# Kernel optimization log

Measured on AMD Instinct MI355X. Metric: run time of the kernel, lower is better.

## Reference

```python
import jax, jax.numpy as jnp
import numpy as np


def _att(xf, W1, W2):
    # xf: [B, L, dk]; low-rank attention scores, softmax over last dim
    dk = W1.shape[0]
    s1 = xf @ W1                                   # [B, L, 10]
    s2 = jnp.einsum('rk,bjk->brj', W2, xf)         # [B, 10, L]
    scores = jnp.einsum('bir,brj->bij', s1, s2) / jnp.sqrt(jnp.float32(dk))
    return jax.nn.softmax(scores, axis=-1)         # [B, L, L]


def setup_inputs() -> dict:
    B, Ci, Co, N, T = 8, 64, 64, 1000, 24
    ks = jax.random.split(jax.random.key(0), 16)
    f32 = jnp.float32
    return {
        'x': jax.random.normal(ks[0], (B, Ci, N, T), f32),
        'A_adj': jax.random.uniform(ks[1], (N, N), f32),
        'att0_W1': jax.random.normal(ks[2], (N * T, 10), f32) * 0.02,
        'att0_W2': jax.random.normal(ks[3], (10, N * T), f32) * 0.02,
        'gatt_W1': jax.random.normal(ks[4], (Ci * T, 10), f32) * 0.02,
        'gatt_W2': jax.random.normal(ks[5], (10, Ci * T), f32) * 0.02,
        'gcn_W': jax.random.normal(ks[6], (Ci, Co), f32) * 0.05,
        'tatt_W1': jax.random.normal(ks[7], (N * Co, 10), f32) * 0.02,
        'tatt_W2': jax.random.normal(ks[8], (10, N * Co), f32) * 0.02,
        'conv1_w': jax.random.normal(ks[9], (Co, Co, 1, 2), f32) * 0.05,
        'conv1_b': jax.random.normal(ks[10], (Co,), f32) * 0.05,
        'conv2_w': jax.random.normal(ks[11], (Co, Co, 1, 2), f32) * 0.05,
        'conv2_b': jax.random.normal(ks[12], (Co,), f32) * 0.05,
        'res_w': jax.random.normal(ks[13], (Co, Ci, 1, 1), f32) * 0.05,
        'res_b': jax.random.normal(ks[14], (Co,), f32) * 0.05,
        'ln_g': jnp.ones((Co,), f32),
        'ln_b': jnp.zeros((Co,), f32),
    }


def reference(x, A_adj, att0_W1, att0_W2, gatt_W1, gatt_W2, gcn_W,
              tatt_W1, tatt_W2, conv1_w, conv1_b, conv2_w, conv2_b,
              res_w, res_b, ln_g, ln_b):
    B, C, N, T = x.shape
    # ---- block-level channel attention (requires_value=True) ----
    xf = x.reshape(B, C, N * T)
    x1 = (_att(xf, att0_W1, att0_W2) @ xf).reshape(B, C, N, T)
    # ---- GCN block: attention-gated adjacency + graph matmul ----
    xg = jnp.transpose(x1, (0, 2, 1, 3)).reshape(B, N, C * T)
    Ag = _att(xg, gatt_W1, gatt_W2) * A_adj                  # [B, N, N]
    g1 = jnp.einsum('bnm,bcmt->bnct', Ag, x1)                # [B, N, C, T]
    g = jnp.einsum('bnct,co->bont', g1, gcn_W)               # [B, Co, N, T]
    Co = g.shape[1]
    # ---- TCN block: temporal attention + dilated causal convs ----
    xt = jnp.transpose(g, (0, 3, 2, 1)).reshape(B, T, N * Co)
    x2 = (_att(xt, tatt_W1, tatt_W2) @ xt).reshape(B, T, N, Co)
    x2 = jnp.transpose(x2, (0, 3, 2, 1))                     # [B, Co, N, T]
    for w, b, d in ((conv1_w, conv1_b, 1), (conv2_w, conv2_b, 2)):
        y = jax.lax.conv_general_dilated(
            x2, w, (1, 1), [(0, 0), (d, d)], rhs_dilation=(1, d),
            dimension_numbers=('NCHW', 'OIHW', 'NCHW'))
        y = y + b[None, :, None, None]
        x2 = jax.nn.relu(y[..., :-d])                        # trim to T
    # ---- 1x1 residual conv ----
    res = jnp.einsum('bcnt,oc->bont', x, res_w[:, :, 0, 0]) + res_b[None, :, None, None]
    out = jax.nn.relu(x2 + res)
    # ---- LayerNorm over channel dim ----
    o = jnp.transpose(out, (0, 3, 2, 1))                     # [B, T, N, Co]
    mu = o.mean(-1, keepdims=True)
    var = o.var(-1, keepdims=True)
    o = (o - mu) / jnp.sqrt(var + 1e-5) * ln_g + ln_b
    return jnp.transpose(o, (0, 3, 2, 1))                    # [B, Co, N, T]
```

## Files before the change

kernel.cpp:

```cpp
#include <hip/hip_runtime.h>
#include <hip/hip_bf16.h>

typedef unsigned int u32;
typedef unsigned short ushortt;

#define B_  8
#define C_  64
#define N_  1000
#define T_  24
#define R_  10
#define NT_ 24000
#define CT_ 1536
#define NC_ 64000

typedef __attribute__((ext_vector_type(8))) short bf8v;
typedef __attribute__((ext_vector_type(4))) float f4v;

__device__ __forceinline__ ushortt f2b_bits(float f) {
  u32 x = __float_as_uint(f);
  u32 r = (x + 0x7fffu + ((x >> 16) & 1u)) >> 16;
  return (ushortt)r;
}

__device__ __forceinline__ u32 f2b_pair(float a, float b) {
  return (u32)f2b_bits(a) | ((u32)f2b_bits(b) << 16);
}

__device__ __forceinline__ float blockSum256(float v, float* red) {
  red[threadIdx.x] = v; __syncthreads();
  #pragma unroll
  for (int s = 128; s > 0; s >>= 1) {
    if (threadIdx.x < s) red[threadIdx.x] += red[threadIdx.x + s];
    __syncthreads();
  }
  float r = red[0]; __syncthreads();
  return r;
}
__device__ __forceinline__ float blockMax256(float v, float* red) {
  red[threadIdx.x] = v; __syncthreads();
  #pragma unroll
  for (int s = 128; s > 0; s >>= 1) {
    if (threadIdx.x < s) red[threadIdx.x] = fmaxf(red[threadIdx.x], red[threadIdx.x + s]);
    __syncthreads();
  }
  float r = red[0]; __syncthreads();
  return r;
}

__global__ __launch_bounds__(256) void zerok(float* p, int n) {
  int i = blockIdx.x * 256 + threadIdx.x;
  if (i < n) p[i] = 0.f;
}

__global__ __launch_bounds__(256) void pack_w(
    const float* __restrict__ W1, const float* __restrict__ W2,
    float* __restrict__ Wp, int K) {
  int i = blockIdx.x * 256 + threadIdx.x;
  if (i >= K * 20) return;
  int k = i / 20, r = i - k * 20;
  Wp[i] = (r < 10) ? W1[(size_t)k * 10 + r] : W2[(size_t)(r - 10) * K + k];
}

__global__ __launch_bounds__(256) void pack_tailw(
    const float* __restrict__ c1w, const float* __restrict__ c2w,
    const float* __restrict__ rw, ushortt* __restrict__ Wt) {
  int i = blockIdx.x * 256 + threadIdx.x;
  if (i >= 20480) return;
  float v;
  if (i < 8192) {
    int tap = i >> 12, o = (i >> 6) & 63, c = i & 63;
    v = c1w[(size_t)(o * 64 + c) * 2 + (tap ? 0 : 1)];
  } else if (i < 16384) {
    int j = i - 8192;
    int tap = j >> 12, o = (j >> 6) & 63, c = j & 63;
    v = c2w[(size_t)(o * 64 + c) * 2 + (tap ? 0 : 1)];
  } else {
    int j = i - 16384;
    v = rw[j];
  }
  Wt[i] = f2b_bits(v);
}

__global__ __launch_bounds__(256) void att0_s12(
    const float* __restrict__ x, const float* __restrict__ Wp,
    float* __restrict__ s1, float* __restrict__ s2) {
  __shared__ float red[40 * 257];
  const int row0 = blockIdx.x * 4;
  const int kbase = blockIdx.y * 6000;
  const int tid = threadIdx.x;
  float acc[4][20];
  #pragma unroll
  for (int r = 0; r < 4; ++r)
    #pragma unroll
    for (int j = 0; j < 20; ++j) acc[r][j] = 0.f;
  const float* xb = x + (size_t)row0 * NT_ + kbase;
  const float4* wb4 = (const float4*)Wp + (size_t)kbase * 5;
  #pragma unroll 1
  for (int it = 0; it < 6; ++it) {
    int slot = tid + 256 * it;
    if (slot < 1500) {
      int k = slot * 4;
      float4 xv0 = *(const float4*)&xb[k];
      float4 xv1 = *(const float4*)&xb[NT_ + k];
      float4 xv2 = *(const float4*)&xb[2 * NT_ + k];
      float4 xv3 = *(const float4*)&xb[3 * NT_ + k];
      const float4* w4 = wb4 + (size_t)slot * 20;
      #pragma unroll
      for (int kk = 0; kk < 4; ++kk) {
        float4 wa = w4[kk * 5 + 0], wbv = w4[kk * 5 + 1], wc = w4[kk * 5 + 2],
               wd = w4[kk * 5 + 3], we = w4[kk * 5 + 4];
        float w[20] = {wa.x,wa.y,wa.z,wa.w, wbv.x,wbv.y,wbv.z,wbv.w,
                       wc.x,wc.y,wc.z,wc.w, wd.x,wd.y,wd.z,wd.w,
                       we.x,we.y,we.z,we.w};
        float xs0 = ((const float*)&xv0)[kk];
        float xs1 = ((const float*)&xv1)[kk];
        float xs2 = ((const float*)&xv2)[kk];
        float xs3 = ((const float*)&xv3)[kk];
        #pragma unroll
        for (int j = 0; j < 20; ++j) {
          acc[0][j] += xs0 * w[j];
          acc[1][j] += xs1 * w[j];
          acc[2][j] += xs2 * w[j];
          acc[3][j] += xs3 * w[j];
        }
      }
    }
  }
  #pragma unroll
  for (int half = 0; half < 2; ++half) {
    __syncthreads();
    #pragma unroll
    for (int mm = 0; mm < 40; ++mm) {
      int m = half * 40 + mm;
      red[mm * 257 + tid] = acc[m / 20][m % 20];
    }
    __syncthreads();
    #pragma unroll
    for (int s = 128; s >= 8; s >>= 1) {
      for (int i = tid; i < 40 * s; i += 256) {
        int rr = i / s, col = i - rr * s;
        red[rr * 257 + col] += red[rr * 257 + col + s];
      }
      __syncthreads();
    }
    if (tid < 40) {
      float v = 0.f;
      #pragma unroll
      for (int c = 0; c < 8; ++c) v += red[tid * 257 + c];
      int m = half * 40 + tid;
      int row = row0 + m / 20, j = m % 20;
      if (j < 10) atomicAdd(&s1[row * 10 + j], v);
      else        atomicAdd(&s2[row * 10 + (j - 10)], v);
    }
  }
}

__global__ __launch_bounds__(64) void att0_softmax(
    const float* __restrict__ s1, const float* __restrict__ s2, float* __restrict__ P) {
  int b = blockIdx.x, i = threadIdx.x;
  float r1[R_];
  #pragma unroll
  for (int r = 0; r < R_; ++r) r1[r] = s1[(b * 64 + i) * R_ + r];
  const float scale = rsqrtf(24000.f);
  float row[64]; float m = -1e30f;
  for (int j = 0; j < 64; ++j) {
    const float* s2r = s2 + (size_t)(b * 64 + j) * R_;
    float d = 0.f;
    #pragma unroll
    for (int r = 0; r < R_; ++r) d += r1[r] * s2r[r];
    d *= scale; row[j] = d; m = fmaxf(m, d);
  }
  float s = 0.f;
  for (int j = 0; j < 64; ++j) { float e = __expf(row[j] - m); row[j] = e; s += e; }
  float inv = 1.f / s;
  for (int j = 0; j < 64; ++j) P[((size_t)b * 64 + i) * 64 + j] = row[j] * inv;
}

__global__ __launch_bounds__(256) void att0_apply(
    const float* __restrict__ x, const float* __restrict__ P, float* __restrict__ x1tr) {
  __shared__ float Pss[4160];
  __shared__ float xt[6144];
  int b = blockIdx.y, n0 = blockIdx.x * 4;
  int tid = threadIdx.x;
  for (int i = tid; i < 4096; i += 256)
    Pss[(i >> 6) * 65 + (i & 63)] = P[(size_t)b * 4096 + i];
  {
    const float4* src4 = (const float4*)x;
    float4* dst4 = (float4*)xt;
    for (int i = tid; i < 1536; i += 256) {
      int j = i / 24, q = i - j * 24;
      dst4[i] = src4[(size_t)(b * 64 + j) * 6000 + n0 * 6 + q];
    }
  }
  __syncthreads();
  int ig = tid >> 4, ln = (tid >> 2) & 3, ts = tid & 3;
  float acc[4][6];
  #pragma unroll
  for (int ii = 0; ii < 4; ++ii)
    #pragma unroll
    for (int m = 0; m < 6; ++m) acc[ii][m] = 0.f;
  const float* base = &xt[ln * 24 + ts * 6];
  #pragma unroll 4
  for (int j = 0; j < 64; ++j) {
    float vj[6];
    #pragma unroll
    for (int m = 0; m < 6; ++m) vj[m] = base[j * 96 + m];
    #pragma unroll
    for (int ii = 0; ii < 4; ++ii) {
      float p = Pss[(ig * 4 + ii) * 65 + j];
      #pragma unroll
      for (int m = 0; m < 6; ++m) acc[ii][m] += p * vj[m];
    }
  }
  float* drow = x1tr + ((size_t)b * N_ + n0 + ln) * CT_ + ts * 6;
  #pragma unroll
  for (int ii = 0; ii < 4; ++ii) {
    float* d = drow + (ig * 4 + ii) * 24;
    *(float2*)&d[0] = make_float2(acc[ii][0], acc[ii][1]);
    *(float2*)&d[2] = make_float2(acc[ii][2], acc[ii][3]);
    *(float2*)&d[4] = make_float2(acc[ii][4], acc[ii][5]);
  }
}

__global__ __launch_bounds__(256) void transpose_x1(
    const float* __restrict__ x1tr, ushortt* __restrict__ Xbt) {
  __shared__ float s[64][65];
  int b = blockIdx.z, n0 = blockIdx.y * 64, c0 = blockIdx.x * 64;
  int tid = threadIdx.x;
  int r = tid >> 2, cc = (tid & 3) * 16;
  if (n0 + r < N_) {
    const float* src = x1tr + ((size_t)b * N_ + n0 + r) * CT_ + c0 + cc;
    #pragma unroll
    for (int i = 0; i < 16; i += 4) {
      float4 v = *(const float4*)&src[i];
      s[r][cc + i] = v.x; s[r][cc + i + 1] = v.y;
      s[r][cc + i + 2] = v.z; s[r][cc + i + 3] = v.w;
    }
  } else {
    #pragma unroll
    for (int i = 0; i < 16; ++i) s[r][cc + i] = 0.f;
  }
  __syncthreads();
  ushortt* dst = Xbt + ((size_t)b * CT_ + c0 + r) * 1024 + n0 + cc;
  #pragma unroll
  for (int i = 0; i < 16; ++i) dst[i] = f2b_bits(s[cc + i][r]);
}

__global__ __launch_bounds__(256) void gatt_s12(
    const float* __restrict__ xg, const float* __restrict__ Wp,
    float* __restrict__ s1, float* __restrict__ s2T) {
  __shared__ float xs[6144];
  __shared__ float red[5120];
  int bn0 = blockIdx.x * 4;
  int tid = threadIdx.x;
  {
    const float4* src4 = (const float4*)(xg + (size_t)bn0 * CT_);
    float4* dst4 = (float4*)xs;
    for (int i = tid; i < 1536; i += 256) dst4[i] = src4[i];
  }
  __syncthreads();
  int rid = tid >> 6, ks = tid & 63;
  float a[20];
  #pragma unroll
  for (int r = 0; r < 20; ++r) a[r] = 0.f;
  for (int k = ks; k < CT_; k += 64) {
    float xv = xs[rid * CT_ + k];
    const float4* wp4 = (const float4*)&Wp[(size_t)k * 20];
    float4 wa = wp4[0], wb = wp4[1], wc = wp4[2], wd = wp4[3], we = wp4[4];
    float wv[20] = {wa.x,wa.y,wa.z,wa.w, wb.x,wb.y,wb.z,wb.w, wc.x,wc.y,wc.z,wc.w,
                    wd.x,wd.y,wd.z,wd.w, we.x,we.y,we.z,we.w};
    #pragma unroll
    for (int r = 0; r < 20; ++r) a[r] += xv * wv[r];
  }
  #pragma unroll
  for (int r = 0; r < 20; ++r) red[tid * 20 + r] = a[r];
  __syncthreads();
  if (tid < 80) {
    int rid2 = tid / 20, r = tid % 20;
    float s = 0.f;
    for (int l = 0; l < 64; ++l) s += red[(rid2 * 64 + l) * 20 + r];
    int row = bn0 + rid2;
    int b = row / N_, n = row - b * N_;
    if (r < 10) s1[row * 10 + r] = s;
    else        s2T[((size_t)b * 10 + (r - 10)) * N_ + n] = s;
  }
}

__global__ __launch_bounds__(256) void gatt_scores(
    const float* __restrict__ s1, const float* __restrict__ s2T,
    const float* __restrict__ Aadj, ushortt* __restrict__ Agb) {
  __shared__ float p[N_];
  __shared__ float r1[R_];
  __shared__ float red[256];
  int b = blockIdx.x / N_, n = blockIdx.x % N_;
  if (threadIdx.x < R_) r1[threadIdx.x] = s1[((size_t)b * N_ + n) * R_ + threadIdx.x];
  __syncthreads();
  const float scale = rsqrtf(1536.f);
  const float* s2b = s2T + (size_t)b * 10 * N_;
  float lmax = -1e30f;
  for (int m = threadIdx.x; m < N_; m += 256) {
    float d = 0.f;
    #pragma unroll
    for (int r = 0; r < R_; ++r) d += r1[r] * s2b[r * N_ + m];
    d *= scale; p[m] = d; lmax = fmaxf(lmax, d);
  }
  float gmax = blockMax256(lmax, red);
  float lsum = 0.f;
  for (int m = threadIdx.x; m < N_; m += 256) {
    float e = __expf(p[m] - gmax); p[m] = e; lsum += e;
  }
  float gsum = blockSum256(lsum, red);
  float inv = 1.f / gsum;
  ushortt* agr = Agb + ((size_t)b * 1024 + n) * 1024;
  const float* ar = Aadj + (size_t)n * N_;
  for (int m = threadIdx.x; m < 1024; m += 256) {
    float v = (m < N_) ? p[m] * inv * ar[m] : 0.f;
    agr[m] = f2b_bits(v);
  }
}

__global__ __launch_bounds__(256) void gemm_mfma(
    const ushortt* __restrict__ Agb, const ushortt* __restrict__ Xbt,
    float* __restrict__ g1) {
  __shared__ ushortt As[2][4096];
  __shared__ ushortt Bs[2][4096];
  const int b = blockIdx.z;
  const int n0 = blockIdx.x * 128;
  const int m0 = blockIdx.y * 128;
  const ushortt* Ab = Agb + (size_t)b * 1024 * 1024;
  const ushortt* Bb = Xbt + (size_t)b * 1536 * 1024;
  const int tid = threadIdx.x;
  const int wave = tid >> 6, lane = tid & 63;
  const int wr = (wave >> 1) * 64, wc = (wave & 1) * 64;
  const int lrow = lane >> 2;
  const int lcol = (lane & 3) * 8;
  const int q = lane >> 4, l15 = lane & 15;

  f4v acc[4][4];
  #pragma unroll
  for (int i = 0; i < 4; ++i)
    #pragma unroll
    for (int j = 0; j < 4; ++j) acc[i][j] = (f4v){0.f, 0.f, 0.f, 0.f};

  const ushortt* gA = Ab + (size_t)(m0 + wave * 16 + lrow) * 1024 + lcol;
  const ushortt* gB = Bb + (size_t)(n0 + wave * 16 + lrow) * 1024 + lcol;

#define GM_STAGE(buf, kk)                                                     \
  do {                                                                        \
    __builtin_amdgcn_global_load_lds(                                         \
      (const __attribute__((address_space(1))) void*)(gA + (kk)),             \
      (__attribute__((address_space(3))) void*)(&As[buf][wave * 512]), 16, 0, 0); \
    __builtin_amdgcn_global_load_lds(                                         \
      (const __attribute__((address_space(1))) void*)(gA + (size_t)64 * 1024 + (kk)), \
      (__attribute__((address_space(3))) void*)(&As[buf][wave * 512 + 2048]), 16, 0, 0); \
    __builtin_amdgcn_global_load_lds(                                         \
      (const __attribute__((address_space(1))) void*)(gB + (kk)),             \
      (__attribute__((address_space(3))) void*)(&Bs[buf][wave * 512]), 16, 0, 0); \
    __builtin_amdgcn_global_load_lds(                                         \
      (const __attribute__((address_space(1))) void*)(gB + (size_t)64 * 1024 + (kk)), \
      (__attribute__((address_space(3))) void*)(&Bs[buf][wave * 512 + 2048]), 16, 0, 0); \
  } while (0)

  GM_STAGE(0, 0);
  __syncthreads();
  int cur = 0;
  for (int k0 = 0; k0 < 1024; k0 += 32) {
    int nxt = cur ^ 1;
    if (k0 + 32 < 1024) GM_STAGE(nxt, k0 + 32);
    bf8v af[4], bfr[4];
    #pragma unroll
    for (int i = 0; i < 4; ++i)
      af[i] = *(const bf8v*)&As[cur][(wr + i * 16 + l15) * 32 + q * 8];
    #pragma unroll
    for (int j = 0; j < 4; ++j)
      bfr[j] = *(const bf8v*)&Bs[cur][(wc + j * 16 + l15) * 32 + q * 8];
    #pragma unroll
    for (int i = 0; i < 4; ++i)
      #pragma unroll
      for (int j = 0; j < 4; ++j)
        acc[i][j] = __builtin_amdgcn_mfma_f32_16x16x32_bf16(af[i], bfr[j], acc[i][j], 0, 0, 0);
    __syncthreads();
    cur = nxt;
  }
#undef GM_STAGE
  #pragma unroll
  for (int i = 0; i < 4; ++i) {
    int rbase = m0 + wr + i * 16 + q * 4;
    #pragma unroll
    for (int r = 0; r < 4; ++r) {
      int gm = rbase + r;
      if (gm < N_) {
        float* dst = g1 + ((size_t)b * N_ + gm) * CT_ + n0 + wc + l15;
        #pragma unroll
        for (int j = 0; j < 4; ++j) dst[j * 16] = acc[i][j][r];
      }
    }
  }
}

__global__ __launch_bounds__(256) void gcn_out(
    const float* __restrict__ g1, const float* __restrict__ W, float* __restrict__ g) {
  __shared__ float gs[6160];
  __shared__ float Ws[4096];
  int b = blockIdx.y, n0 = blockIdx.x * 4;
  int tid = threadIdx.x;
  {
    const float4* src4 = (const float4*)g1;
    float4* dst4 = (float4*)gs;
    for (int i = tid; i < 1536; i += 256) {
      int ln = i / 384, q = i - ln * 384;
      dst4[ln * 385 + q] = src4[(size_t)(b * N_ + n0 + ln) * 384 + q];
    }
  }
  for (int i = tid; i < 4096; i += 256) Ws[i] = W[i];
  __syncthreads();
  int og = tid >> 4, ln = (tid >> 2) & 3, ts = tid & 3;
  float acc[4][6];
  #pragma unroll
  for (int oo = 0; oo < 4; ++oo)
    #pragma unroll
    for (int m = 0; m < 6; ++m) acc[oo][m] = 0.f;
  const float* base = &gs[ln * 1540 + ts * 6];
  #pragma unroll 4
  for (int c = 0; c < 64; ++c) {
    float v[6];
    #pragma unroll
    for (int m = 0; m < 6; ++m) v[m] = base[c * 24 + m];
    float4 w4 = *(const float4*)&Ws[c * 64 + og * 4];
    float wv[4] = {w4.x, w4.y, w4.z, w4.w};
    #pragma unroll
    for (int oo = 0; oo < 4; ++oo)
      #pragma unroll
      for (int m = 0; m < 6; ++m) acc[oo][m] += wv[oo] * v[m];
  }
  #pragma unroll
  for (int oo = 0; oo < 4; ++oo) {
    int o = og * 4 + oo;
    float* d = g + (((size_t)(b * C_ + o)) * N_ + n0 + ln) * T_ + ts * 6;
    *(float2*)&d[0] = make_float2(acc[oo][0], acc[oo][1]);
    *(float2*)&d[2] = make_float2(acc[oo][2], acc[oo][3]);
    *(float2*)&d[4] = make_float2(acc[oo][4], acc[oo][5]);
  }
}

__global__ __launch_bounds__(256) void tatt_s12(
    const float* __restrict__ g, const float* __restrict__ Wp,
    float* __restrict__ s1, float* __restrict__ s2) {
  __shared__ float red[40 * 257];
  const int b = blockIdx.z, t0 = blockIdx.y * 4, n0 = blockIdx.x * 20;
  const int tid = threadIdx.x;
  const int o = tid & 63, nl = tid >> 6;
  float acc[4][20];
  #pragma unroll
  for (int tt = 0; tt < 4; ++tt)
    #pragma unroll
    for (int j = 0; j < 20; ++j) acc[tt][j] = 0.f;
  const float* gb = g + (size_t)(b * 64 + o) * NT_ + t0;
  #pragma unroll 1
  for (int it = 0; it < 5; ++it) {
    int n = n0 + it * 4 + nl;
    float4 gv = *(const float4*)&gb[n * 24];
    const float4* w4 = (const float4*)&Wp[(size_t)(n * 64 + o) * 20];
    float4 wa = w4[0], wbv = w4[1], wc = w4[2], wd = w4[3], we = w4[4];
    float w[20] = {wa.x,wa.y,wa.z,wa.w, wbv.x,wbv.y,wbv.z,wbv.w,
                   wc.x,wc.y,wc.z,wc.w, wd.x,wd.y,wd.z,wd.w,
                   we.x,we.y,we.z,we.w};
    float gs[4] = {gv.x, gv.y, gv.z, gv.w};
    #pragma unroll
    for (int tt = 0; tt < 4; ++tt)
      #pragma unroll
      for (int j = 0; j < 20; ++j) acc[tt][j] += gs[tt] * w[j];
  }
  #pragma unroll
  for (int half = 0; half < 2; ++half) {
    __syncthreads();
    #pragma unroll
    for (int mm = 0; mm < 40; ++mm) {
      int m = half * 40 + mm;
      red[mm * 257 + tid] = acc[m / 20][m % 20];
    }
    __syncthreads();
    #pragma unroll
    for (int s = 128; s >= 8; s >>= 1) {
      for (int i = tid; i < 40 * s; i += 256) {
        int rr = i / s, col = i - rr * s;
        red[rr * 257 + col] += red[rr * 257 + col + s];
      }
      __syncthreads();
    }
    if (tid < 40) {
      float v = 0.f;
      #pragma unroll
      for (int c = 0; c < 8; ++c) v += red[tid * 257 + c];
      int m = half * 40 + tid;
      int t = t0 + m / 20, j = m % 20;
      if (j < 10) atomicAdd(&s1[(b * T_ + t) * R_ + j], v);
      else        atomicAdd(&s2[(b * T_ + t) * R_ + (j - 10)], v);
    }
  }
}

__global__ __launch_bounds__(64) void tatt_softmax(
    const float* __restrict__ s1, const float* __restrict__ s2, float* __restrict__ Pt) {
  int b = blockIdx.x, t = threadIdx.x;
  if (t >= T_) return;
  float r1[R_];
  #pragma unroll
  for (int r = 0; r < R_; ++r) r1[r] = s1[(b * T_ + t) * R_ + r];
  const float scale = rsqrtf(64000.f);
  float row[T_]; float m = -1e30f;
  for (int j = 0; j < T_; ++j) {
    const float* s2r = s2 + (b * T_ + j) * R_;
    float d = 0.f;
    #pragma unroll
    for (int r = 0; r < R_; ++r) d += r1[r] * s2r[r];
    d *= scale; row[j] = d; m = fmaxf(m, d);
  }
  float s = 0.f;
  for (int j = 0; j < T_; ++j) { float e = __expf(row[j] - m); row[j] = e; s += e; }
  float inv = 1.f / s;
  for (int j = 0; j < T_; ++j) Pt[(b * T_ + t) * T_ + j] = row[j] * inv;
}

#define CSB 1024
#define RSB 104
#define PFS 66
__global__ __launch_bounds__(256, 4) void tail_k(
    const float* __restrict__ g, const float* __restrict__ Pt,
    const float* __restrict__ x,
    const ushortt* __restrict__ Wt,
    const float* __restrict__ c1b, const float* __restrict__ c2b,
    const float* __restrict__ rb,
    const float* __restrict__ lg, const float* __restrict__ lb,
    float* __restrict__ outp) {
  __shared__ __align__(16) ushortt LSH[16384];
  __shared__ __align__(16) float PtS[576];
  __shared__ float mu[96], rs[96];
  ushortt* L0 = LSH;
  ushortt* L1 = LSH + 8192;
  float* preF = (float*)LSH;
  int b = blockIdx.y, n0 = blockIdx.x * 4;
  int tid = threadIdx.x;
  int wave = tid >> 6, lane = tid & 63;
  int q = lane >> 4, l15 = lane & 15;

  if (tid < 144)
    ((float4*)PtS)[tid] = ((const float4*)(Pt + (size_t)b * 576))[tid];
  const int sc = tid >> 2, snl = tid & 3;
  float gr[24];
  {
    const float4* gp = (const float4*)(g + ((size_t)(b * 64 + sc) * 1000 + n0 + snl) * 24);
    #pragma unroll
    for (int q2 = 0; q2 < 6; ++q2) {
      float4 v = gp[q2];
      gr[q2 * 4] = v.x; gr[q2 * 4 + 1] = v.y; gr[q2 * 4 + 2] = v.z; gr[q2 * 4 + 3] = v.w;
    }
  }
  #pragma unroll
  for (int rep = 0; rep < 6; ++rep) {
    int i = tid + rep * 256;
    int c = i / 24, qq = i - c * 24;
    const float4* src = (const float4*)(x + ((size_t)(b * 64 + c) * 1000 + n0) * 24);
    float4 v = src[qq];
    *(uint2*)&L1[c * RSB + qq * 4] = make_uint2(f2b_pair(v.x, v.y), f2b_pair(v.z, v.w));
  }
  __syncthreads();

  {
    u32 w12[12];
    #pragma unroll
    for (int t = 0; t < 24; t += 2) {
      float a0 = 0.f, a1 = 0.f;
      const float4* p0 = (const float4*)&PtS[t * 24];
      const float4* p1 = (const float4*)&PtS[t * 24 + 24];
      #pragma unroll
      for (int q2 = 0; q2 < 6; ++q2) {
        float4 v0 = p0[q2], v1 = p1[q2];
        a0 += v0.x * gr[q2 * 4] + v0.y * gr[q2 * 4 + 1]
            + v0.z * gr[q2 * 4 + 2] + v0.w * gr[q2 * 4 + 3];
        a1 += v1.x * gr[q2 * 4] + v1.y * gr[q2 * 4 + 1]
            + v1.z * gr[q2 * 4 + 2] + v1.w * gr[q2 * 4 + 3];
      }
      w12[t >> 1] = f2b_pair(a0, a1);
    }
    uint4* da = (uint4*)&L0[sc * RSB + snl * 24];
    da[0] = make_uint4(w12[0], w12[1], w12[2], w12[3]);
    da[1] = make_uint4(w12[4], w12[5], w12[6], w12[7]);
    da[2] = make_uint4(w12[8], w12[9], w12[10], w12[11]);
  }
  __syncthreads();

  u32 pa[4][4];
  int sKblk[4], sCol[4];
  #pragma unroll
  for (int rep = 0; rep < 4; ++rep) {
    int slot = tid + rep * 256;
    int kblk = slot >> 7, col = slot & 127;
    sKblk[rep] = kblk; sCol[rep] = col;
    int nl2 = col >> 5, s = col & 31;
    if (s >= 2 && s <= 25) {
      int boff = (kblk * 8) * RSB + nl2 * 24 + (s - 2);
      #pragma unroll
      for (int h = 0; h < 4; ++h) {
        u32 a0 = L0[boff + (2 * h) * RSB], a1 = L0[boff + (2 * h + 1) * RSB];
        pa[rep][h] = a0 | (a1 << 16);
      }
    } else {
      #pragma unroll
      for (int h = 0; h < 4; ++h) pa[rep][h] = 0u;
    }
  }
  __syncthreads();
  #pragma unroll
  for (int rep = 0; rep < 4; ++rep)
    *(uint4*)&L0[sKblk[rep] * CSB + sCol[rep] * 8] =
        make_uint4(pa[rep][0], pa[rep][1], pa[rep][2], pa[rep][3]);
  __syncthreads();

  f4v acc1[2][4];
  #pragma unroll
  for (int ct = 0; ct < 2; ++ct)
    #pragma unroll
    for (int mt = 0; mt < 4; ++mt) acc1[ct][mt] = (f4v){0.f, 0.f, 0.f, 0.f};
  #pragma unroll
  for (int ki = 0; ki < 2; ++ki) {
    bf8v a0[4], a1[4];
    #pragma unroll
    for (int mt = 0; mt < 4; ++mt) {
      a0[mt] = *(const bf8v*)&Wt[(mt * 16 + l15) * 64 + ki * 32 + q * 8];
      a1[mt] = *(const bf8v*)&Wt[4096 + (mt * 16 + l15) * 64 + ki * 32 + q * 8];
    }
    #pragma unroll
    for (int ct = 0; ct < 2; ++ct) {
      int col = wave * 32 + ct * 16 + l15;
      int colp = (col == 0) ? 0 : col - 1;
      bf8v bc = *(const bf8v*)&L0[(ki * 4 + q) * CSB + col * 8];
      bf8v bp = *(const bf8v*)&L0[(ki * 4 + q) * CSB + colp * 8];
      #pragma unroll
      for (int mt = 0; mt < 4; ++mt) {
        acc1[ct][mt] = __builtin_amdgcn_mfma_f32_16x16x32_bf16(a0[mt], bc, acc1[ct][mt], 0, 0, 0);
        acc1[ct][mt] = __builtin_amdgcn_mfma_f32_16x16x32_bf16(a1[mt], bp, acc1[ct][mt], 0, 0, 0);
      }
    }
  }
  u32 kb[4][4];
  #pragma unroll
  for (int rep = 0; rep < 4; ++rep) {
    int col = sCol[rep];
    int nl2 = col >> 5, s = col & 31;
    if (s >= 2 && s <= 25) {
      int boff = (sKblk[rep] * 8) * RSB + nl2 * 24 + (s - 2);
      #pragma unroll
      for (int h = 0; h < 4; ++h) {
        u32 b0 = L1[boff + (2 * h) * RSB], b1 = L1[boff + (2 * h + 1) * RSB];
        kb[rep][h] = b0 | (b1 << 16);
      }
    } else {
      #pragma unroll
      for (int h = 0; h < 4; ++h) kb[rep][h] = 0u;
    }
  }
  u32 ypack[2][4][2];
  #pragma unroll
  for (int ct = 0; ct < 2; ++ct) {
    int s = ct * 16 + l15;
    bool v = (s >= 2 && s <= 25);
    #pragma unroll
    for (int mt = 0; mt < 4; ++mt) {
      int o0 = mt * 16 + q * 4;
      float4 bb = *(const float4*)&c1b[o0];
      float y0 = v ? fmaxf(acc1[ct][mt][0] + bb.x, 0.f) : 0.f;
      float y1 = v ? fmaxf(acc1[ct][mt][1] + bb.y, 0.f) : 0.f;
      float y2 = v ? fmaxf(acc1[ct][mt][2] + bb.z, 0.f) : 0.f;
      float y3 = v ? fmaxf(acc1[ct][mt][3] + bb.w, 0.f) : 0.f;
      ypack[ct][mt][0] = f2b_pair(y0, y1);
      ypack[ct][mt][1] = f2b_pair(y2, y3);
    }
  }
  __syncthreads();

  #pragma unroll
  for (int ct = 0; ct < 2; ++ct) {
    int col = wave * 32 + ct * 16 + l15;
    #pragma unroll
    for (int mt = 0; mt < 4; ++mt) {
      int o0 = mt * 16 + q * 4;
      *(uint2*)&L0[(o0 >> 3) * CSB + col * 8 + (o0 & 7)] =
          make_uint2(ypack[ct][mt][0], ypack[ct][mt][1]);
    }
  }
  #pragma unroll
  for (int rep = 0; rep < 4; ++rep)
    *(uint4*)&L1[sKblk[rep] * CSB + sCol[rep] * 8] =
        make_uint4(kb[rep][0], kb[rep][1], kb[rep][2], kb[rep][3]);
  __syncthreads();

  f4v accA[2][4], accR[2][4];
  #pragma unroll
  for (int ct = 0; ct < 2; ++ct)
    #pragma unroll
    for (int mt = 0; mt < 4; ++mt) {
      accA[ct][mt] = (f4v){0.f, 0.f, 0.f, 0.f};
      accR[ct][mt] = (f4v){0.f, 0.f, 0.f, 0.f};
    }
  #pragma unroll
  for (int ki = 0; ki < 2; ++ki) {
    bf8v c0[4], c1t[4], rrf[4];
    #pragma unroll
    for (int mt = 0; mt < 4; ++mt) {
      c0[mt]  = *(const bf8v*)&Wt[8192 + (mt * 16 + l15) * 64 + ki * 32 + q * 8];
      c1t[mt] = *(const bf8v*)&Wt[12288 + (mt * 16 + l15) * 64 + ki * 32 + q * 8];
      rrf[mt] = *(const bf8v*)&Wt[16384 + (mt * 16 + l15) * 64 + ki * 32 + q * 8];
    }
    #pragma unroll
    for (int ct = 0; ct < 2; ++ct) {
      int col = wave * 32 + ct * 16 + l15;
      int colp2 = (col < 2) ? col : col - 2;
      bf8v bc = *(const bf8v*)&L0[(ki * 4 + q) * CSB + col * 8];
      bf8v bp = *(const bf8v*)&L0[(ki * 4 + q) * CSB + colp2 * 8];
      bf8v bx = *(const bf8v*)&L1[(ki * 4 + q) * CSB + col * 8];
      #pragma unroll
      for (int mt = 0; mt < 4; ++mt) {
        accA[ct][mt] = __builtin_amdgcn_mfma_f32_16x16x32_bf16(c0[mt], bc, accA[ct][mt], 0, 0, 0);
        accA[ct][mt] = __builtin_amdgcn_mfma_f32_16x16x32_bf16(c1t[mt], bp, accA[ct][mt], 0, 0, 0);
        accR[ct][mt] = __builtin_amdgcn_mfma_f32_16x16x32_bf16(rrf[mt], bx, accR[ct][mt], 0, 0, 0);
      }
    }
  }
  float pre[2][4][4];
  #pragma unroll
  for (int ct = 0; ct < 2; ++ct) {
    #pragma unroll
    for (int mt = 0; mt < 4; ++mt) {
      int o0 = mt * 16 + q * 4;
      float4 b2 = *(const float4*)&c2b[o0];
      float4 rbv = *(const float4*)&rb[o0];
      float bb2[4] = {b2.x, b2.y, b2.z, b2.w};
      float brv[4] = {rbv.x, rbv.y, rbv.z, rbv.w};
      #pragma unroll
      for (int r = 0; r < 4; ++r) {
        float a = fmaxf(accA[ct][mt][r] + bb2[r], 0.f) + accR[ct][mt][r] + brv[r];
        pre[ct][mt][r] = fmaxf(a, 0.f);
      }
    }
  }
  __syncthreads();

  #pragma unroll
  for (int ct = 0; ct < 2; ++ct) {
    int s = ct * 16 + l15;
    if (s >= 2 && s <= 25) {
      int p = wave * 24 + s - 2;
      #pragma unroll
      for (int mt = 0; mt < 4; ++mt) {
        int o0 = mt * 16 + q * 4;
        *(float2*)&preF[p * PFS + o0]     = make_float2(pre[ct][mt][0], pre[ct][mt][1]);
        *(float2*)&preF[p * PFS + o0 + 2] = make_float2(pre[ct][mt][2], pre[ct][mt][3]);
      }
    }
  }
  __syncthreads();
  if (tid < 96) {
    const float* pr = &preF[tid * PFS];
    float sm = 0.f, qq = 0.f;
    #pragma unroll 16
    for (int c = 0; c < 64; ++c) {
      float v = pr[c];
      sm += v; qq += v * v;
    }
    float m = sm * (1.f / 64.f);
    mu[tid] = m;
    rs[tid] = rsqrtf(qq * (1.f / 64.f) - m * m + 1e-5f);
  }
  __syncthreads();
  {
    int o = tid >> 2, nl = tid & 3;
    float gam = lg[o], bet = lb[o];
    float vals[24];
    #pragma unroll
    for (int t = 0; t < 24; ++t) {
      int p = nl * 24 + t;
      vals[t] = (preF[p * PFS + o] - mu[p]) * rs[p] * gam + bet;
    }
    float* dst = outp + ((size_t)(b * 64 + o) * 1000 + n0 + nl) * 24;
    #pragma unroll
    for (int t = 0; t < 24; t += 4)
      *(float4*)&dst[t] = make_float4(vals[t], vals[t+1], vals[t+2], vals[t+3]);
  }
}

extern "C" void kernel_launch(void* const* d_in, const int* in_sizes, int n_in,
                              void* d_out, int out_size, void* d_ws, size_t ws_size,
                              hipStream_t stream) {
  const float* x     = (const float*)d_in[0];
  const float* Aadj  = (const float*)d_in[1];
  const float* a0W1  = (const float*)d_in[2];
  const float* a0W2  = (const float*)d_in[3];
  const float* gW1   = (const float*)d_in[4];
  const float* gW2   = (const float*)d_in[5];
  const float* gcnW  = (const float*)d_in[6];
  const float* tW1   = (const float*)d_in[7];
  const float* tW2   = (const float*)d_in[8];
  const float* c1w   = (const float*)d_in[9];
  const float* c1b   = (const float*)d_in[10];
  const float* c2w   = (const float*)d_in[11];
  const float* c2b   = (const float*)d_in[12];
  const float* rw    = (const float*)d_in[13];
  const float* rb    = (const float*)d_in[14];
  const float* lng   = (const float*)d_in[15];
  const float* lnb   = (const float*)d_in[16];
  float* out = (float*)d_out;

  float* ws = (float*)d_ws;
  float* R1   = ws;
  float* U    = R1 + 12288000;
  float* D    = U + 12288000;
  float* s1_0 = D + 12288000;
  float* s2_0 = s1_0 + 5120;
  float* P0   = s2_0 + 5120;
  float* s1g  = P0 + 32768;
  float* s2gT = s1g + 80000;
  float* s1t  = s2gT + 80000;
  float* s2t  = s1t + 1920;
  float* Ptb  = s2t + 1920;
  float* Wp0  = Ptb + 4608;
  float* Wgp  = Wp0 + 480000;
  float* Wtp  = Wgp + 30720;
  float* Wtl  = Wtp + 1280000;
  ushortt* Xbt = (ushortt*)U;
  ushortt* Agb = (ushortt*)(U + 6291456);
  ushortt* Wtail = (ushortt*)Wtl;
  float* g = U;
  if (ws_size < (size_t)38876416 * 4) return;

  pack_w<<<1875, 256, 0, stream>>>(a0W1, a0W2, Wp0, 24000);
  pack_w<<<120, 256, 0, stream>>>(gW1, gW2, Wgp, 1536);
  pack_w<<<5000, 256, 0, stream>>>(tW1, tW2, Wtp, 64000);
  pack_tailw<<<80, 256, 0, stream>>>(c1w, c2w, rw, Wtail);
  zerok<<<40, 256, 0, stream>>>(s1_0, 10240);
  att0_s12<<<dim3(128, 4), 256, 0, stream>>>(x, Wp0, s1_0, s2_0);
  att0_softmax<<<8, 64, 0, stream>>>(s1_0, s2_0, P0);
  att0_apply<<<dim3(250, 8), 256, 0, stream>>>(x, P0, R1);
  gatt_s12<<<2000, 256, 0, stream>>>(R1, Wgp, s1g, s2gT);
  transpose_x1<<<dim3(24, 16, 8), 256, 0, stream>>>(R1, Xbt);
  gatt_scores<<<8000, 256, 0, stream>>>(s1g, s2gT, Aadj, Agb);
  gemm_mfma<<<dim3(12, 8, 8), 256, 0, stream>>>(Agb, Xbt, D);
  gcn_out<<<dim3(250, 8), 256, 0, stream>>>(D, gcnW, g);
  zerok<<<15, 256, 0, stream>>>(s1t, 3840);
  tatt_s12<<<dim3(50, 6, 8), 256, 0, stream>>>(g, Wtp, s1t, s2t);
  tatt_softmax<<<8, 32, 0, stream>>>(s1t, s2t, Ptb);
  tail_k<<<dim3(250, 8), 256, 0, stream>>>(g, Ptb, x, Wtail,
                                           c1b, c2b, rb, lng, lnb, out);
}
```

Measured before the change: 521.0 us.

## Fuse gatt score projection into att0_apply and store x1 as bf16

Merges the graph-attention s1/s2 projection into the att0_apply kernel, so the x1 tile is reused from shared memory instead of being written out and read back as fp32. The intermediate x1 is now written as bf16, which halves the write and the later read by transpose_x1, and the transpose now moves bf16 values directly. This saves one kernel launch and roughly 150 MB of fp32 traffic. In exchange, shared memory per block grows through aliased buffers, and the x1 values fed to the GEMM are rounded to bf16 before the transpose; the old path also converted them to bf16 there, so the result is unchanged.

```diff
diff --git a/kernel.cpp b/kernel.cpp
--- a/kernel.cpp
+++ b/kernel.cpp
@@ -176,10 +176,15 @@
   for (int j = 0; j < 64; ++j) P[((size_t)b * 64 + i) * 64 + j] = row[j] * inv;
 }
 
-__global__ __launch_bounds__(256) void att0_apply(
-    const float* __restrict__ x, const float* __restrict__ P, float* __restrict__ x1tr) {
-  __shared__ float Pss[4160];
-  __shared__ float xt[6144];
+__global__ __launch_bounds__(256) void att0_apply_gatt(
+    const float* __restrict__ x, const float* __restrict__ P,
+    const float* __restrict__ Wgp,
+    ushortt* __restrict__ x1b, float* __restrict__ s1g, float* __restrict__ s2gT) {
+  __shared__ float SH[11264];
+  float* Pss = SH;
+  float* xt  = SH + 5120;
+  float* red = SH;
+  float* xs  = SH + 5120;
   int b = blockIdx.y, n0 = blockIdx.x * 4;
   int tid = threadIdx.x;
   for (int i = tid; i < 4096; i += 256)
@@ -212,78 +217,72 @@
       for (int m = 0; m < 6; ++m) acc[ii][m] += p * vj[m];
     }
   }
-  float* drow = x1tr + ((size_t)b * N_ + n0 + ln) * CT_ + ts * 6;
-  #pragma unroll
-  for (int ii = 0; ii < 4; ++ii) {
-    float* d = drow + (ig * 4 + ii) * 24;
-    *(float2*)&d[0] = make_float2(acc[ii][0], acc[ii][1]);
-    *(float2*)&d[2] = make_float2(acc[ii][2], acc[ii][3]);
-    *(float2*)&d[4] = make_float2(acc[ii][4], acc[ii][5]);
+  __syncthreads();
+  {
+    ushortt* drow = x1b + ((size_t)b * N_ + n0 + ln) * CT_ + ts * 6;
+    float* xrow = &xs[ln * CT_ + ts * 6];
+    #pragma unroll
+    for (int ii = 0; ii < 4; ++ii) {
+      int ctb = (ig * 4 + ii) * 24;
+      #pragma unroll
+      for (int m = 0; m < 6; ++m) xrow[ctb + m] = acc[ii][m];
+      *(u32*)&drow[ctb]     = f2b_pair(acc[ii][0], acc[ii][1]);
+      *(u32*)&drow[ctb + 2] = f2b_pair(acc[ii][2], acc[ii][3]);
+      *(u32*)&drow[ctb + 4] = f2b_pair(acc[ii][4], acc[ii][5]);
+    }
+  }
+  __syncthreads();
+  int rid = tid >> 6, ks = tid & 63;
+  float a[20];
+  #pragma unroll
+  for (int r = 0; r < 20; ++r) a[r] = 0.f;
+  for (int k = ks; k < CT_; k += 64) {
+    float xv = xs[rid * CT_ + k];
+    const float4* wp4 = (const float4*)&Wgp[(size_t)k * 20];
+    float4 wa = wp4[0], wb = wp4[1], wc = wp4[2], wd = wp4[3], we = wp4[4];
+    float wv[20] = {wa.x,wa.y,wa.z,wa.w, wb.x,wb.y,wb.z,wb.w, wc.x,wc.y,wc.z,wc.w,
+                    wd.x,wd.y,wd.z,wd.w, we.x,we.y,we.z,we.w};
+    #pragma unroll
+    for (int r = 0; r < 20; ++r) a[r] += xv * wv[r];
+  }
+  #pragma unroll
+  for (int r = 0; r < 20; ++r) red[tid * 20 + r] = a[r];
+  __syncthreads();
+  if (tid < 80) {
+    int rid2 = tid / 20, r = tid % 20;
+    float s = 0.f;
+    for (int l = 0; l < 64; ++l) s += red[(rid2 * 64 + l) * 20 + r];
+    int n = n0 + rid2;
+    int row = b * N_ + n;
+    if (r < 10) s1g[row * 10 + r] = s;
+    else        s2gT[((size_t)b * 10 + (r - 10)) * N_ + n] = s;
   }
 }
 
 __global__ __launch_bounds__(256) void transpose_x1(
-    const float* __restrict__ x1tr, ushortt* __restrict__ Xbt) {
-  __shared__ float s[64][65];
+    const ushortt* __restrict__ x1b, ushortt* __restrict__ Xbt) {
+  __shared__ ushortt st[64][66];
   int b = blockIdx.z, n0 = blockIdx.y * 64, c0 = blockIdx.x * 64;
   int tid = threadIdx.x;
   int r = tid >> 2, cc = (tid & 3) * 16;
   if (n0 + r < N_) {
-    const float* src = x1tr + ((size_t)b * N_ + n0 + r) * CT_ + c0 + cc;
-    #pragma unroll
-    for (int i = 0; i < 16; i += 4) {
-      float4 v = *(const float4*)&src[i];
-      s[r][cc + i] = v.x; s[r][cc + i + 1] = v.y;
-      s[r][cc + i + 2] = v.z; s[r][cc + i + 3] = v.w;
-    }
+    const ushortt* src = x1b + ((size_t)b * N_ + n0 + r) * CT_ + c0 + cc;
+    ushortt tmp[16];
+    *(uint4*)&tmp[0] = *(const uint4*)&src[0];
+    *(uint4*)&tmp[8] = *(const uint4*)&src[8];
+    #pragma unroll
+    for (int i = 0; i < 16; ++i) st[r][cc + i] = tmp[i];
   } else {
     #pragma unroll
-    for (int i = 0; i < 16; ++i) s[r][cc + i] = 0.f;
-  }
-  __syncthreads();
+    for (int i = 0; i < 16; ++i) st[r][cc + i] = 0;
+  }
+  __syncthreads();
+  ushortt out[16];
+  #pragma unroll
+  for (int i = 0; i < 16; ++i) out[i] = st[cc + i][r];
   ushortt* dst = Xbt + ((size_t)b * CT_ + c0 + r) * 1024 + n0 + cc;
-  #pragma unroll
-  for (int i = 0; i < 16; ++i) dst[i] = f2b_bits(s[cc + i][r]);
-}
-
-__global__ __launch_bounds__(256) void gatt_s12(
-    const float* __restrict__ xg, const float* __restrict__ Wp,
-    float* __restrict__ s1, float* __restrict__ s2T) {
-  __shared__ float xs[6144];
-  __shared__ float red[5120];
-  int bn0 = blockIdx.x * 4;
-  int tid = threadIdx.x;
-  {
-    const float4* src4 = (const float4*)(xg + (size_t)bn0 * CT_);
-    float4* dst4 = (float4*)xs;
-    for (int i = tid; i < 1536; i += 256) dst4[i] = src4[i];
-  }
-  __syncthreads();
-  int rid = tid >> 6, ks = tid & 63;
-  float a[20];
-  #pragma unroll
-  for (int r = 0; r < 20; ++r) a[r] = 0.f;
-  for (int k = ks; k < CT_; k += 64) {
-    float xv = xs[rid * CT_ + k];
-    const float4* wp4 = (const float4*)&Wp[(size_t)k * 20];
-    float4 wa = wp4[0], wb = wp4[1], wc = wp4[2], wd = wp4[3], we = wp4[4];
-    float wv[20] = {wa.x,wa.y,wa.z,wa.w, wb.x,wb.y,wb.z,wb.w, wc.x,wc.y,wc.z,wc.w,
-                    wd.x,wd.y,wd.z,wd.w, we.x,we.y,we.z,we.w};
-    #pragma unroll
-    for (int r = 0; r < 20; ++r) a[r] += xv * wv[r];
-  }
-  #pragma unroll
-  for (int r = 0; r < 20; ++r) red[tid * 20 + r] = a[r];
-  __syncthreads();
-  if (tid < 80) {
-    int rid2 = tid / 20, r = tid % 20;
-    float s = 0.f;
-    for (int l = 0; l < 64; ++l) s += red[(rid2 * 64 + l) * 20 + r];
-    int row = bn0 + rid2;
-    int b = row / N_, n = row - b * N_;
-    if (r < 10) s1[row * 10 + r] = s;
-    else        s2T[((size_t)b * 10 + (r - 10)) * N_ + n] = s;
-  }
+  *(uint4*)&dst[0] = *(const uint4*)&out[0];
+  *(uint4*)&dst[8] = *(const uint4*)&out[8];
 }
 
 __global__ __launch_bounds__(256) void gatt_scores(
@@ -827,6 +826,7 @@
   float* Wgp  = Wp0 + 480000;
   float* Wtp  = Wgp + 30720;
   float* Wtl  = Wtp + 1280000;
+  ushortt* x1b = (ushortt*)R1;
   ushortt* Xbt = (ushortt*)U;
   ushortt* Agb = (ushortt*)(U + 6291456);
   ushortt* Wtail = (ushortt*)Wtl;
@@ -840,9 +840,8 @@
   zerok<<<40, 256, 0, stream>>>(s1_0, 10240);
   att0_s12<<<dim3(128, 4), 256, 0, stream>>>(x, Wp0, s1_0, s2_0);
   att0_softmax<<<8, 64, 0, stream>>>(s1_0, s2_0, P0);
-  att0_apply<<<dim3(250, 8), 256, 0, stream>>>(x, P0, R1);
-  gatt_s12<<<2000, 256, 0, stream>>>(R1, Wgp, s1g, s2gT);
-  transpose_x1<<<dim3(24, 16, 8), 256, 0, stream>>>(R1, Xbt);
+  att0_apply_gatt<<<dim3(250, 8), 256, 0, stream>>>(x, P0, Wgp, x1b, s1g, s2gT);
+  transpose_x1<<<dim3(24, 16, 8), 256, 0, stream>>>(x1b, Xbt);
   gatt_scores<<<8000, 256, 0, stream>>>(s1g, s2gT, Aadj, Agb);
   gemm_mfma<<<dim3(12, 8, 8), 256, 0, stream>>>(Agb, Xbt, D);
   gcn_out<<<dim3(250, 8), 256, 0, stream>>>(D, gcnW, g);
```

Measured after the change: 496.0 us. -4.8%, faster.
